# Performance work log

Measured on AMD Instinct MI355X. Metric: run time of the kernel, lower is better.

## Reference

```python
import jax, jax.numpy as jnp
import numpy as np

NUM_TILES = 512
N_POINTS = 512
D_IN = 256
D_OUT = 256
CHANNELS = 1024


def setup_inputs() -> dict:
    key = jax.random.key(0)
    k1, k2, k3 = jax.random.split(key, 3)
    x = jax.random.normal(k1, (NUM_TILES, N_POINTS, D_IN), dtype=jnp.float32)
    indices = jax.random.randint(k2, (NUM_TILES,), 0, CHANNELS, dtype=jnp.int64)
    # kaiming-uniform-like init for the per-channel weight tiles
    bound = float(np.sqrt(6.0 / D_IN))
    weight = jax.random.uniform(k3, (CHANNELS, D_IN, D_OUT), dtype=jnp.float32,
                                minval=-bound, maxval=bound)
    bias = jnp.zeros((1, 1, D_OUT), dtype=jnp.float32)
    return {"x": x, "indices": indices, "weight": weight, "bias": bias}


def reference(x, indices, weight, bias):
    # gather per-tile weights [T, D_in, D_out], then batched matmul
    w = weight[indices]  # [T, D_in, D_out]
    # [T, P, D_in] @ [T, D_in, D_out] -> [T, P, D_out]
    out = jnp.einsum('tpi,tio->tpo', x, w) + bias[0]
    return out
```

## Files before the change

kernel.cpp:

```cpp
#include <hip/hip_runtime.h>
#include <hip/hip_bf16.h>

typedef __attribute__((ext_vector_type(8))) short bf16x8;
typedef __attribute__((ext_vector_type(4))) short bf16x4;
typedef __attribute__((ext_vector_type(4))) float f32x4;

constexpr int NT   = 512;
constexpr int NP   = 512;
constexpr int DIN  = 256;
constexpr int DOUT = 256;
constexpr int BN   = 128;
constexpr int CHM  = 32;
constexpr int NEP  = NP / CHM;

__device__ __forceinline__ short f2bf(float f) {
  __hip_bfloat16 h = __float2bfloat16(f);
  return __builtin_bit_cast(short, h);
}

__device__ __forceinline__ void wg_barrier() {
  asm volatile("s_waitcnt lgkmcnt(0)" ::: "memory");
  __builtin_amdgcn_s_barrier();
  __builtin_amdgcn_sched_barrier(0);
}

__device__ __forceinline__ int wsw(int n, int k) {
  return n * DIN + (k ^ (((n ^ (n >> 2)) & 7) << 3));
}

__device__ __forceinline__ int xsw(int m, int k) {
  return m * DIN + (k ^ ((m & 7) << 3));
}

__global__ __launch_bounds__(512, 4) void adaptive_linear_v12(
    const float* __restrict__ x,
    const int*   __restrict__ idx,
    const float* __restrict__ w,
    const float* __restrict__ bias,
    float*       __restrict__ out)
{
  __shared__ short Ws[BN * DIN];
  __shared__ short Xs[CHM * DIN];

  const int tid = threadIdx.x;
  const int b   = blockIdx.x;
  const int t   = (b >> 4) * 8 + (b & 7);
  const int nh  = (b >> 3) & 1;

  const int c = idx[t];
  const float* xb = x   + (size_t)t * NP * DIN;
  const float* wb = w   + (size_t)c * DIN * DOUT + nh * BN;
  float*       ob = out + (size_t)t * NP * DOUT + nh * BN;

  {
    const int n4 = (tid & 31) * 4;
    const int kg = tid >> 5;
    f32x4 wr[4];
    #pragma unroll 1
    for (int ss = 0; ss < 4; ++ss) {
      const int k0 = ss * 64 + kg * 4;
      const float* src = wb + (size_t)k0 * DOUT + n4;
      #pragma unroll
      for (int r = 0; r < 4; ++r)
        wr[r] = *reinterpret_cast<const f32x4*>(src + (size_t)r * DOUT);
      #pragma unroll
      for (int j = 0; j < 4; ++j) {
        bf16x4 v = { f2bf(wr[0][j]), f2bf(wr[1][j]),
                     f2bf(wr[2][j]), f2bf(wr[3][j]) };
        *reinterpret_cast<bf16x4*>(&Ws[wsw(n4 + j, k0)]) = v;
      }
    }
  }

  f32x4 xr[4];
  auto load_x = [&](int e) {
    const float* base = xb + (size_t)e * CHM * DIN;
    #pragma unroll
    for (int i = 0; i < 4; ++i)
      xr[i] = *reinterpret_cast<const f32x4*>(base + i * 2048 + tid * 4);
  };
  auto write_x = [&]() {
    const int m0 = tid >> 6;
    const int k  = (tid & 63) * 4;
    #pragma unroll
    for (int i = 0; i < 4; ++i) {
      bf16x4 v = { f2bf(xr[i][0]), f2bf(xr[i][1]),
                   f2bf(xr[i][2]), f2bf(xr[i][3]) };
      *reinterpret_cast<bf16x4*>(&Xs[xsw(m0 + i * 8, k)]) = v;
    }
  };

  const int l    = tid & 63;
  const int wid  = tid >> 6;
  const int wm   = wid >> 2;
  const int wn   = wid & 3;
  const int lrow = l & 15;
  const int lk   = l >> 4;

  float bv[2];
  #pragma unroll
  for (int fn = 0; fn < 2; ++fn)
    bv[fn] = bias[nh * BN + wn * 32 + fn * 16 + lrow];

  load_x(0);
  write_x();
  wg_barrier();

  for (int e = 0; e < NEP; ++e) {
    if (e < NEP - 1) load_x(e + 1);

    f32x4 acc[2][2] = {};
    #pragma unroll
    for (int ks = 0; ks < 8; ++ks) {
      const int kb = ks * 32 + lk * 8;
      bf16x8 a[2], bb[2];
      #pragma unroll
      for (int fm = 0; fm < 2; ++fm)
        a[fm] = *reinterpret_cast<const bf16x8*>(
            &Xs[xsw(wm * 16 + fm * 8, kb)]);
      a[0] = *reinterpret_cast<const bf16x8*>(&Xs[xsw(wm * 16 + lrow, kb)]);
      #pragma unroll
      for (int fn = 0; fn < 2; ++fn)
        bb[fn] = *reinterpret_cast<const bf16x8*>(
            &Ws[wsw(wn * 32 + fn * 16 + lrow, kb)]);
      #pragma unroll
      for (int fn = 0; fn < 2; ++fn)
        acc[0][fn] = __builtin_amdgcn_mfma_f32_16x16x32_bf16(
            a[0], bb[fn], acc[0][fn], 0, 0, 0);
    }

    {
      const int r0w = e * CHM + wm * 16 + lk * 4;
      #pragma unroll
      for (int fn = 0; fn < 2; ++fn) {
        const int col = wn * 32 + fn * 16 + lrow;
        float* op = ob + (size_t)r0w * DOUT + col;
        #pragma unroll
        for (int rr = 0; rr < 4; ++rr)
          op[(size_t)rr * DOUT] = acc[0][fn][rr] + bv[fn];
      }
    }

    if (e < NEP - 1) {
      wg_barrier();
      write_x();
      wg_barrier();
    }
  }
}

extern "C" void kernel_launch(void* const* d_in, const int* in_sizes, int n_in,
                              void* d_out, int out_size, void* d_ws, size_t ws_size,
                              hipStream_t stream) {
  const float* x    = (const float*)d_in[0];
  const int*   idx  = (const int*)d_in[1];
  const float* w    = (const float*)d_in[2];
  const float* bias = (const float*)d_in[3];
  float* out = (float*)d_out;

  adaptive_linear_v12<<<NT * 2, 512, 0, stream>>>(x, idx, w, bias, out);
}
```

Before: 145.6 us.

## Warp-specialize producer/consumer waves with double-buffered X tile

Splits the block into four producer waves that load and convert X rows into a double-buffered LDS tile, and four consumer waves that each compute a full 16x128 output strip with MFMA. The chunk size doubles to 64 rows, which halves the number of barriers and lets the next tile load overlap compute. The cost is that half the waves do no MFMA work, register use per thread rises (16 f32x4 loads or 8 accumulators), LDS grows, and occupancy drops to 2 blocks per CU.

New measurement: 129.4 us. 1.13x faster.

```diff
diff --git a/kernel.cpp b/kernel.cpp
--- a/kernel.cpp
+++ b/kernel.cpp
@@ -10,7 +10,7 @@
 constexpr int DIN  = 256;
 constexpr int DOUT = 256;
 constexpr int BN   = 128;
-constexpr int CHM  = 32;
+constexpr int CHM  = 64;
 constexpr int NEP  = NP / CHM;
 
 __device__ __forceinline__ short f2bf(float f) {
@@ -32,7 +32,7 @@
   return m * DIN + (k ^ ((m & 7) << 3));
 }
 
-__global__ __launch_bounds__(512, 4) void adaptive_linear_v12(
+__global__ __launch_bounds__(512, 2) void adaptive_linear_v13(
     const float* __restrict__ x,
     const int*   __restrict__ idx,
     const float* __restrict__ w,
@@ -40,7 +40,7 @@
     float*       __restrict__ out)
 {
   __shared__ short Ws[BN * DIN];
-  __shared__ short Xs[CHM * DIN];
+  __shared__ short Xs[2][CHM * DIN];
 
   const int tid = threadIdx.x;
   const int b   = blockIdx.x;
@@ -51,6 +51,9 @@
   const float* xb = x   + (size_t)t * NP * DIN;
   const float* wb = w   + (size_t)c * DIN * DOUT + nh * BN;
   float*       ob = out + (size_t)t * NP * DOUT + nh * BN;
+
+  const int l   = tid & 63;
+  const int wid = tid >> 6;
 
   {
     const int n4 = (tid & 31) * 4;
@@ -72,80 +75,71 @@
     }
   }
 
-  f32x4 xr[4];
+  const bool producer = (wid < 4);
+  const int  p = wid;
+  const int  q = wid - 4;
+
+  f32x4 xr[16];
   auto load_x = [&](int e) {
-    const float* base = xb + (size_t)e * CHM * DIN;
+    const float* base = xb + (size_t)e * CHM * DIN + (size_t)(p * 16) * DIN + l * 4;
     #pragma unroll
-    for (int i = 0; i < 4; ++i)
-      xr[i] = *reinterpret_cast<const f32x4*>(base + i * 2048 + tid * 4);
+    for (int i = 0; i < 16; ++i)
+      xr[i] = *reinterpret_cast<const f32x4*>(base + (size_t)i * DIN);
   };
-  auto write_x = [&]() {
-    const int m0 = tid >> 6;
-    const int k  = (tid & 63) * 4;
+  auto write_x = [&](int buf) {
     #pragma unroll
-    for (int i = 0; i < 4; ++i) {
+    for (int i = 0; i < 16; ++i) {
       bf16x4 v = { f2bf(xr[i][0]), f2bf(xr[i][1]),
                    f2bf(xr[i][2]), f2bf(xr[i][3]) };
-      *reinterpret_cast<bf16x4*>(&Xs[xsw(m0 + i * 8, k)]) = v;
+      *reinterpret_cast<bf16x4*>(&Xs[buf][xsw(p * 16 + i, l * 4)]) = v;
     }
   };
 
-  const int l    = tid & 63;
-  const int wid  = tid >> 6;
-  const int wm   = wid >> 2;
-  const int wn   = wid & 3;
   const int lrow = l & 15;
   const int lk   = l >> 4;
+  float bv[8];
+  if (!producer) {
+    #pragma unroll
+    for (int j = 0; j < 8; ++j)
+      bv[j] = bias[nh * BN + j * 16 + lrow];
+  }
 
-  float bv[2];
-  #pragma unroll
-  for (int fn = 0; fn < 2; ++fn)
-    bv[fn] = bias[nh * BN + wn * 32 + fn * 16 + lrow];
-
-  load_x(0);
-  write_x();
+  if (producer) load_x(0);
+  if (producer) write_x(0);
   wg_barrier();
 
   for (int e = 0; e < NEP; ++e) {
-    if (e < NEP - 1) load_x(e + 1);
-
-    f32x4 acc[2][2] = {};
-    #pragma unroll
-    for (int ks = 0; ks < 8; ++ks) {
-      const int kb = ks * 32 + lk * 8;
-      bf16x8 a[2], bb[2];
+    if (producer) {
+      if (e < NEP - 1) {
+        load_x(e + 1);
+        write_x((e + 1) & 1);
+      }
+    } else {
+      f32x4 acc[8] = {};
+      const short* xbuf = Xs[e & 1];
       #pragma unroll
-      for (int fm = 0; fm < 2; ++fm)
-        a[fm] = *reinterpret_cast<const bf16x8*>(
-            &Xs[xsw(wm * 16 + fm * 8, kb)]);
-      a[0] = *reinterpret_cast<const bf16x8*>(&Xs[xsw(wm * 16 + lrow, kb)]);
+      for (int ks = 0; ks < 8; ++ks) {
+        const int kb = ks * 32 + lk * 8;
+        const bf16x8 a = *reinterpret_cast<const bf16x8*>(
+            &xbuf[xsw(q * 16 + lrow, kb)]);
+        #pragma unroll
+        for (int j = 0; j < 8; ++j) {
+          const bf16x8 bb = *reinterpret_cast<const bf16x8*>(
+              &Ws[wsw(j * 16 + lrow, kb)]);
+          acc[j] = __builtin_amdgcn_mfma_f32_16x16x32_bf16(a, bb, acc[j], 0, 0, 0);
+        }
+      }
+      const int r0w = e * CHM + q * 16 + lk * 4;
       #pragma unroll
-      for (int fn = 0; fn < 2; ++fn)
-        bb[fn] = *reinterpret_cast<const bf16x8*>(
-            &Ws[wsw(wn * 32 + fn * 16 + lrow, kb)]);
-      #pragma unroll
-      for (int fn = 0; fn < 2; ++fn)
-        acc[0][fn] = __builtin_amdgcn_mfma_f32_16x16x32_bf16(
-            a[0], bb[fn], acc[0][fn], 0, 0, 0);
-    }
-
-    {
-      const int r0w = e * CHM + wm * 16 + lk * 4;
-      #pragma unroll
-      for (int fn = 0; fn < 2; ++fn) {
-        const int col = wn * 32 + fn * 16 + lrow;
+      for (int j = 0; j < 8; ++j) {
+        const int col = j * 16 + lrow;
         float* op = ob + (size_t)r0w * DOUT + col;
         #pragma unroll
         for (int rr = 0; rr < 4; ++rr)
-          op[(size_t)rr * DOUT] = acc[0][fn][rr] + bv[fn];
+          op[(size_t)rr * DOUT] = acc[j][rr] + bv[j];
       }
     }
-
-    if (e < NEP - 1) {
-      wg_barrier();
-      write_x();
-      wg_barrier();
-    }
+    if (e < NEP - 1) wg_barrier();
   }
 }
 
@@ -158,5 +152,5 @@
   const float* bias = (const float*)d_in[3];
   float* out = (float*)d_out;
 
-  adaptive_linear_v12<<<NT * 2, 512, 0, stream>>>(x, idx, w, bias, out);
+  adaptive_linear_v13<<<NT * 2, 512, 0, stream>>>(x, idx, w, bias, out);
 }
```

## Stage x tiles with async global-to-LDS loads into double-buffered fp32 LDS

Applied to the files above, without the earlier changes.

Replaces the register round-trip for x (global load, bf16 convert, LDS store, two barriers) with direct global_load_lds transfers into a double-buffered fp32 LDS tile, swizzled on the source address. The fp32-to-bf16 conversion moves to the MFMA consumer side, and each chunk now needs only one barrier, gated by a vmcnt wait. The aim is to overlap x fetches with compute and cut instruction and barrier overhead. In exchange, LDS use grows from about 80KB to 128KB, which likely leaves one block per CU instead of two. Each wave also repeats the conversion for rows that the other waves sharing them convert too.

New measurement: 175.6 us. 20.6% more time.

```diff
diff --git a/kernel.cpp b/kernel.cpp
--- a/kernel.cpp
+++ b/kernel.cpp
@@ -18,21 +18,22 @@
   return __builtin_bit_cast(short, h);
 }
 
-__device__ __forceinline__ void wg_barrier() {
-  asm volatile("s_waitcnt lgkmcnt(0)" ::: "memory");
-  __builtin_amdgcn_s_barrier();
-  __builtin_amdgcn_sched_barrier(0);
+__device__ __forceinline__ bf16x8 cvt8(f32x4 a, f32x4 b) {
+  bf16x8 r;
+  r[0] = f2bf(a[0]); r[1] = f2bf(a[1]); r[2] = f2bf(a[2]); r[3] = f2bf(a[3]);
+  r[4] = f2bf(b[0]); r[5] = f2bf(b[1]); r[6] = f2bf(b[2]); r[7] = f2bf(b[3]);
+  return r;
 }
 
 __device__ __forceinline__ int wsw(int n, int k) {
   return n * DIN + (k ^ (((n ^ (n >> 2)) & 7) << 3));
 }
 
-__device__ __forceinline__ int xsw(int m, int k) {
-  return m * DIN + (k ^ ((m & 7) << 3));
+__device__ __forceinline__ int xg(int r, int g) {
+  return r * DIN + ((g ^ (r & 7)) << 2);
 }
 
-__global__ __launch_bounds__(512, 4) void adaptive_linear_v12(
+__global__ __launch_bounds__(512, 2) void adaptive_linear_v14(
     const float* __restrict__ x,
     const int*   __restrict__ idx,
     const float* __restrict__ w,
@@ -40,7 +41,7 @@
     float*       __restrict__ out)
 {
   __shared__ short Ws[BN * DIN];
-  __shared__ short Xs[CHM * DIN];
+  __shared__ float Xf[2][CHM * DIN];
 
   const int tid = threadIdx.x;
   const int b   = blockIdx.x;
@@ -51,6 +52,21 @@
   const float* xb = x   + (size_t)t * NP * DIN;
   const float* wb = w   + (size_t)c * DIN * DOUT + nh * BN;
   float*       ob = out + (size_t)t * NP * DOUT + nh * BN;
+
+  const int l   = tid & 63;
+  const int wid = tid >> 6;
+
+  auto stage_x = [&](int e, int buf) {
+    #pragma unroll
+    for (int i = 0; i < 4; ++i) {
+      const int r = wid * 4 + i;
+      const float* src = xb + (size_t)(e * CHM + r) * DIN + ((l ^ (r & 7)) << 2);
+      __builtin_amdgcn_global_load_lds(
+          (const __attribute__((address_space(1))) void*)src,
+          (__attribute__((address_space(3))) void*)&Xf[buf][r * DIN],
+          16, 0, 0);
+    }
+  };
 
   {
     const int n4 = (tid & 31) * 4;
@@ -72,26 +88,6 @@
     }
   }
 
-  f32x4 xr[4];
-  auto load_x = [&](int e) {
-    const float* base = xb + (size_t)e * CHM * DIN;
-    #pragma unroll
-    for (int i = 0; i < 4; ++i)
-      xr[i] = *reinterpret_cast<const f32x4*>(base + i * 2048 + tid * 4);
-  };
-  auto write_x = [&]() {
-    const int m0 = tid >> 6;
-    const int k  = (tid & 63) * 4;
-    #pragma unroll
-    for (int i = 0; i < 4; ++i) {
-      bf16x4 v = { f2bf(xr[i][0]), f2bf(xr[i][1]),
-                   f2bf(xr[i][2]), f2bf(xr[i][3]) };
-      *reinterpret_cast<bf16x4*>(&Xs[xsw(m0 + i * 8, k)]) = v;
-    }
-  };
-
-  const int l    = tid & 63;
-  const int wid  = tid >> 6;
   const int wm   = wid >> 2;
   const int wn   = wid & 3;
   const int lrow = l & 15;
@@ -102,31 +98,28 @@
   for (int fn = 0; fn < 2; ++fn)
     bv[fn] = bias[nh * BN + wn * 32 + fn * 16 + lrow];
 
-  load_x(0);
-  write_x();
-  wg_barrier();
+  stage_x(0, 0);
+  __syncthreads();
 
   for (int e = 0; e < NEP; ++e) {
-    if (e < NEP - 1) load_x(e + 1);
+    if (e < NEP - 1) stage_x(e + 1, (e + 1) & 1);
 
-    f32x4 acc[2][2] = {};
+    f32x4 acc[2] = {};
+    const float* xs = Xf[e & 1];
+    const int r = wm * 16 + lrow;
     #pragma unroll
     for (int ks = 0; ks < 8; ++ks) {
+      const int g0 = ks * 8 + lk * 2;
+      const f32x4 va = *reinterpret_cast<const f32x4*>(&xs[xg(r, g0)]);
+      const f32x4 vb = *reinterpret_cast<const f32x4*>(&xs[xg(r, g0 + 1)]);
+      const bf16x8 a = cvt8(va, vb);
       const int kb = ks * 32 + lk * 8;
-      bf16x8 a[2], bb[2];
       #pragma unroll
-      for (int fm = 0; fm < 2; ++fm)
-        a[fm] = *reinterpret_cast<const bf16x8*>(
-            &Xs[xsw(wm * 16 + fm * 8, kb)]);
-      a[0] = *reinterpret_cast<const bf16x8*>(&Xs[xsw(wm * 16 + lrow, kb)]);
-      #pragma unroll
-      for (int fn = 0; fn < 2; ++fn)
-        bb[fn] = *reinterpret_cast<const bf16x8*>(
+      for (int fn = 0; fn < 2; ++fn) {
+        const bf16x8 bb = *reinterpret_cast<const bf16x8*>(
             &Ws[wsw(wn * 32 + fn * 16 + lrow, kb)]);
-      #pragma unroll
-      for (int fn = 0; fn < 2; ++fn)
-        acc[0][fn] = __builtin_amdgcn_mfma_f32_16x16x32_bf16(
-            a[0], bb[fn], acc[0][fn], 0, 0, 0);
+        acc[fn] = __builtin_amdgcn_mfma_f32_16x16x32_bf16(a, bb, acc[fn], 0, 0, 0);
+      }
     }
 
     {
@@ -137,14 +130,14 @@
         float* op = ob + (size_t)r0w * DOUT + col;
         #pragma unroll
         for (int rr = 0; rr < 4; ++rr)
-          op[(size_t)rr * DOUT] = acc[0][fn][rr] + bv[fn];
+          op[(size_t)rr * DOUT] = acc[fn][rr] + bv[fn];
       }
     }
 
     if (e < NEP - 1) {
-      wg_barrier();
-      write_x();
-      wg_barrier();
+      asm volatile("s_waitcnt vmcnt(8) lgkmcnt(0)" ::: "memory");
+      __builtin_amdgcn_s_barrier();
+      __builtin_amdgcn_sched_barrier(0);
     }
   }
 }
@@ -158,5 +151,5 @@
   const float* bias = (const float*)d_in[3];
   float* out = (float*)d_out;
 
-  adaptive_linear_v12<<<NT * 2, 512, 0, stream>>>(x, idx, w, bias, out);
+  adaptive_linear_v14<<<NT * 2, 512, 0, stream>>>(x, idx, w, bias, out);
 }
```
